# Optimization experiments

Measured on AMD Instinct MI355X. Metric: run time of the kernel, lower is better.

Reference implementation:

```python
import jax, jax.numpy as jnp
import numpy as np

B, T, I, H = 64, 512, 512, 1024

def _xavier(key, shape):
    fan_in, fan_out = shape
    limit = float(np.sqrt(6.0 / (fan_in + fan_out)))
    return jax.random.uniform(key, shape, jnp.float32, -limit, limit)

def setup_inputs() -> dict:
    key = jax.random.key(0)
    ks = jax.random.split(key, 9)
    inp = {
        'x': jax.random.normal(ks[0], (B, T, I), jnp.float32),
        'U_inputgate': _xavier(ks[1], (I, H)),
        'V_inputgate': _xavier(ks[2], (H, H)),
        'bias_inputgate': jnp.zeros((H,), jnp.float32),
        'U_forget': _xavier(ks[3], (I, H)),
        'V_forget': _xavier(ks[4], (H, H)),
        'bias_forget': jnp.zeros((H,), jnp.float32),
        'U_tilded': _xavier(ks[5], (I, H)),
        'V_tilded': _xavier(ks[6], (H, H)),
        'bias_tilded': jnp.zeros((H,), jnp.float32),
        'U_output': _xavier(ks[7], (I, H)),
        'V_output': _xavier(ks[8], (H, H)),
        'bias_output': jnp.zeros((H,), jnp.float32),
    }
    return inp

def reference(x, U_inputgate, V_inputgate, bias_inputgate,
              U_forget, V_forget, bias_forget,
              U_tilded, V_tilded, bias_tilded,
              U_output, V_output, bias_output):
    batch = x.shape[0]
    hidden = V_inputgate.shape[0]
    # Precompute input projections for all timesteps (fused gate GEMM):
    # concat U's -> one [I, 4H] GEMM over the whole sequence.
    U = jnp.concatenate([U_inputgate, U_forget, U_tilded, U_output], axis=1)  # [I, 4H]
    V = jnp.concatenate([V_inputgate, V_forget, V_tilded, V_output], axis=1)  # [H, 4H]
    b = jnp.concatenate([bias_inputgate, bias_forget, bias_tilded, bias_output])  # [4H]
    xU = jnp.einsum('bti,ig->btg', x, U) + b  # [B, T, 4H]

    def step(carry, xu_t):
        h, c = carry
        g = xu_t + h @ V  # [B, 4H]
        i_g = jax.nn.sigmoid(g[:, :hidden])
        f_g = jax.nn.sigmoid(g[:, hidden:2 * hidden])
        c_t = jnp.tanh(g[:, 2 * hidden:3 * hidden])
        o_g = jax.nn.sigmoid(g[:, 3 * hidden:])
        c_new = i_g * c_t + f_g * c
        h_new = o_g * jnp.tanh(c_new)
        return (h_new, c_new), None

    h0 = jnp.zeros((batch, hidden), x.dtype)
    c0 = jnp.zeros((batch, hidden), x.dtype)
    (h_t, c_t), _ = jax.lax.scan(step, (h0, c0), jnp.swapaxes(xU, 0, 1))
    return (h_t, c_t)
```

## Files before the change

### kernel.cpp

```cpp
#include <hip/hip_runtime.h>
#include <hip/hip_bf16.h>
#include <cstdio>
#include <cstdint>

#define BB 64
#define TT 512
#define II 512
#define HH 1024
#define G4H 4096
#define TC 256

typedef __attribute__((ext_vector_type(8))) short short8b;
typedef __attribute__((ext_vector_type(4))) float f32x4;
typedef unsigned long long ull;

union U16 { uint4 u; short8b s; };

#define AT_LD32(p)   __hip_atomic_load((p), __ATOMIC_RELAXED, __HIP_MEMORY_SCOPE_AGENT)
#define AT_LD64(p)   __hip_atomic_load((p), __ATOMIC_RELAXED, __HIP_MEMORY_SCOPE_AGENT)
#define AT_ST32(p,v) __hip_atomic_store((p), (v), __ATOMIC_RELAXED, __HIP_MEMORY_SCOPE_AGENT)
#define AT_ST64(p,v) __hip_atomic_store((p), (v), __ATOMIC_RELAXED, __HIP_MEMORY_SCOPE_AGENT)

__device__ __forceinline__ ushort f2bf(float f) {
    union { float f; unsigned u; } x; x.f = f;
    unsigned r = x.u + 0x7FFFu + ((x.u >> 16) & 1u);
    return (ushort)(r >> 16);
}
__device__ __forceinline__ float bf2f(ushort b) {
    union { unsigned u; float f; } x; x.u = ((unsigned)b) << 16;
    return x.f;
}
__device__ __forceinline__ float sigm(float x) { return 1.f / (1.f + __expf(-x)); }
__device__ __forceinline__ float tanh_(float x) { return 2.f / (1.f + __expf(-2.f * x)) - 1.f; }

__global__ void conv_f32_bf16(const float* __restrict__ in, ushort* __restrict__ out, int n) {
    int i = (blockIdx.x * blockDim.x + threadIdx.x) * 4;
    int stride = gridDim.x * blockDim.x * 4;
    for (; i < n; i += stride) {
        float4 v = *(const float4*)(in + i);
        ushort4 o;
        o.x = f2bf(v.x); o.y = f2bf(v.y); o.z = f2bf(v.z); o.w = f2bf(v.w);
        *(ushort4*)(out + i) = o;
    }
}

__global__ void transpose_bf16(const float* __restrict__ in, ushort* __restrict__ out, int K) {
    __shared__ float tile[32][33];
    int j0 = blockIdx.x * 32;
    int k0 = blockIdx.y * 32;
    int tx = threadIdx.x, ty = threadIdx.y;
    #pragma unroll
    for (int i = 0; i < 32; i += 8)
        tile[ty + i][tx] = in[(size_t)(k0 + ty + i) * 1024 + j0 + tx];
    __syncthreads();
    #pragma unroll
    for (int i = 0; i < 32; i += 8)
        out[(size_t)(j0 + ty + i) * K + k0 + tx] = f2bf(tile[tx][ty + i]);
}

__global__ __launch_bounds__(256) void gemm_xu(
    const ushort* __restrict__ A, const ushort* __restrict__ Bt,
    const float* __restrict__ b0, const float* __restrict__ b1,
    const float* __restrict__ b2, const float* __restrict__ b3,
    ushort* __restrict__ C, int t0)
{
    __shared__ ushort As[128 * 64];
    __shared__ ushort Bs[128 * 64];
    const int m0 = blockIdx.x * 128;
    const int n0 = blockIdx.y * 128;
    const int tid = threadIdx.x;
    const int lane = tid & 63;
    const int wave = tid >> 6;
    const int wm = (wave >> 1) * 64;
    const int wn = (wave & 1) * 64;
    const int kgrp = lane >> 4;

    const ushort* Abase = A + ((size_t)(m0 >> 8) * TT + t0 + (m0 & 255)) * 512;

    f32x4 acc[4][4];
    #pragma unroll
    for (int i = 0; i < 4; ++i)
        #pragma unroll
        for (int j = 0; j < 4; ++j) acc[i][j] = (f32x4){0.f, 0.f, 0.f, 0.f};

    for (int k0 = 0; k0 < 512; k0 += 64) {
        __syncthreads();
        #pragma unroll
        for (int p = 0; p < 4; ++p) {
            int idx = p * 256 + tid;
            int row = idx >> 3;
            int kc  = idx & 7;
            uint4 va = *(const uint4*)(Abase + (size_t)row * 512 + k0 + kc * 8);
            uint4 vb = *(const uint4*)(Bt + (size_t)(n0 + row) * 512 + k0 + kc * 8);
            int bo = (row * 128 + kc * 16) ^ ((row & 7) << 4);
            *(uint4*)((char*)As + bo) = va;
            *(uint4*)((char*)Bs + bo) = vb;
        }
        __syncthreads();
        #pragma unroll
        for (int ks = 0; ks < 2; ++ks) {
            U16 af[4], bfr[4];
            #pragma unroll
            for (int i = 0; i < 4; ++i) {
                int row = wm + i * 16 + (lane & 15);
                int ao = (row * 128 + ks * 64 + kgrp * 16) ^ ((row & 7) << 4);
                af[i].u = *(const uint4*)((const char*)As + ao);
                int col = wn + i * 16 + (lane & 15);
                int bo = (col * 128 + ks * 64 + kgrp * 16) ^ ((col & 7) << 4);
                bfr[i].u = *(const uint4*)((const char*)Bs + bo);
            }
            #pragma unroll
            for (int i = 0; i < 4; ++i)
                #pragma unroll
                for (int j = 0; j < 4; ++j)
                    acc[i][j] = __builtin_amdgcn_mfma_f32_16x16x32_bf16(af[i].s, bfr[j].s, acc[i][j], 0, 0, 0);
        }
    }
    #pragma unroll
    for (int i = 0; i < 4; ++i) {
        #pragma unroll
        for (int j = 0; j < 4; ++j) {
            int row = m0 + wm + i * 16 + (lane >> 4) * 4;
            int col = n0 + wn + j * 16 + (lane & 15);
            int gate = col >> 10;
            const float* bp = (gate == 0) ? b0 : (gate == 1) ? b1 : (gate == 2) ? b2 : b3;
            float bias = bp[col & 1023];
            #pragma unroll
            for (int r = 0; r < 4; ++r)
                C[(size_t)(row + r) * G4H + col] = f2bf(acc[i][j][r] + bias);
        }
    }
}

__global__ __launch_bounds__(256, 1) void lstm_rec(
    const ushort* __restrict__ xU,
    const ushort* __restrict__ V_t,
    char* __restrict__ hb,
    float* __restrict__ cbuf,
    float* __restrict__ out,
    unsigned* __restrict__ flags,
    int t0)
{
    __shared__ __align__(16) ushort Vl[64 * 1024];
    __shared__ __align__(16) ushort hl[16 * 1024];

    const int wgid = blockIdx.x;
    const int grp = wgid >> 6;
    const int slice = wgid & 63;
    const int tid = threadIdx.x;
    const int lane = tid & 63;
    const int w = tid >> 6;

    #pragma unroll
    for (int p = 0; p < 32; ++p) {
        int idx = p * 256 + tid;
        int c  = idx >> 7;
        int kc = idx & 127;
        int colg = (c & 3) * 1024 + slice * 16 + ((c >> 4) << 2) + ((c >> 2) & 3);
        uint4 v = *(const uint4*)(V_t + (size_t)colg * 1024 + kc * 8);
        int bo = (c * 2048 + kc * 16) ^ ((c & 7) << 4);
        *(uint4*)((char*)Vl + bo) = v;
    }

    const int myrow = (lane >> 4) * 4 + (lane & 3);
    const int mycol = 4 * w + ((lane >> 2) & 3);
    const int growf = grp * 16 + myrow;
    const int hcol = slice * 16 + mycol;
    float c_reg = (t0 == 0) ? 0.f : cbuf[(size_t)growf * 1024 + hcol];

    const int kgrp = lane >> 4;
    const int lrow = lane & 15;
    const int arow_sw = (lrow & 7) << 4;
    const int bc = w * 16 + (lane & 15);
    const int bxor = (bc & 7) << 4;
    const int bo_base = bc * 2048 + kgrp * 16;

    __syncthreads();

    for (int t = t0; t < t0 + TC; ++t) {
        size_t xbase = ((size_t)growf * TC + (t - t0)) * G4H + hcol;
        ushort xi = xU[xbase], xf = xU[xbase + 1024], xc = xU[xbase + 2048], xo = xU[xbase + 3072];

        if (tid < 64) {
            const unsigned tgt = (unsigned)t;
            const unsigned* f = flags + grp * 64;
            while (!__all((int)(AT_LD32(&f[tid]) >= tgt)))
                __builtin_amdgcn_s_sleep(1);
            asm volatile("" ::: "memory");
        }
        __syncthreads();

        {
            const char* hsrc = hb + (size_t)(t & 1) * 131072 + grp * 32768;
            ull vv[16];
            #pragma unroll
            for (int it = 0; it < 16; ++it)
                vv[it] = AT_LD64((const ull*)(hsrc + (size_t)(it * 256 + tid) * 8));
            #pragma unroll
            for (int it = 0; it < 16; ++it) {
                int q = it * 256 + tid;
                int row = q >> 8;
                int cb  = (q & 255) * 8;
                *(ull*)((char*)hl + ((row * 2048 + cb) ^ ((row & 7) << 4))) = vv[it];
            }
        }
        __syncthreads();

        f32x4 acc0 = (f32x4){0.f,0.f,0.f,0.f}, acc1 = (f32x4){0.f,0.f,0.f,0.f};
        const char* hlb = (const char*)hl;
        #pragma unroll
        for (int ks = 0; ks < 32; ks += 2) {
            U16 a0, b0, a1, b1;
            a0.u = *(const uint4*)(hlb + ((lrow * 2048 + (ks * 4 + kgrp) * 16) ^ arow_sw));
            b0.u = *(const uint4*)((const char*)Vl + ((bo_base + ks * 64) ^ bxor));
            acc0 = __builtin_amdgcn_mfma_f32_16x16x32_bf16(a0.s, b0.s, acc0, 0, 0, 0);
            a1.u = *(const uint4*)(hlb + ((lrow * 2048 + (ks * 4 + 4 + kgrp) * 16) ^ arow_sw));
            b1.u = *(const uint4*)((const char*)Vl + ((bo_base + ks * 64 + 64) ^ bxor));
            acc1 = __builtin_amdgcn_mfma_f32_16x16x32_bf16(a1.s, b1.s, acc1, 0, 0, 0);
        }
        float a0 = acc0[0] + acc1[0], a1 = acc0[1] + acc1[1];
        float a2 = acc0[2] + acc1[2], a3 = acc0[3] + acc1[3];

        {
            float b0 = __shfl_xor(a1, 1), b1 = __shfl_xor(a0, 1);
            float b2 = __shfl_xor(a3, 1), b3 = __shfl_xor(a2, 1);
            bool o1 = (lane & 1) != 0;
            a0 = o1 ? b0 : a0;  a1 = o1 ? a1 : b1;
            a2 = o1 ? b2 : a2;  a3 = o1 ? a3 : b3;
            b0 = __shfl_xor(a2, 2); b1 = __shfl_xor(a3, 2);
            b2 = __shfl_xor(a0, 2); b3 = __shfl_xor(a1, 2);
            bool o2 = (lane & 2) != 0;
            a0 = o2 ? b0 : a0;  a1 = o2 ? b1 : a1;
            a2 = o2 ? a2 : b2;  a3 = o2 ? a3 : b3;
        }

        float gi = a0 + bf2f(xi), gf = a1 + bf2f(xf);
        float gc = a2 + bf2f(xc), go = a3 + bf2f(xo);
        float ig = sigm(gi), fg = sigm(gf), ct = tanh_(gc), og = sigm(go);
        c_reg = ig * ct + fg * c_reg;
        float h = og * tanh_(c_reg);
        ushort hbf = f2bf(h);
        unsigned h1 = __shfl_down((unsigned)hbf, 4);
        unsigned h2 = __shfl_down((unsigned)hbf, 8);
        unsigned h3 = __shfl_down((unsigned)hbf, 12);
        if (((lane >> 2) & 3) == 0) {
            ull pk = (ull)hbf | ((ull)(h1 & 0xffff) << 16)
                   | ((ull)(h2 & 0xffff) << 32) | ((ull)(h3 & 0xffff) << 48);
            AT_ST64((ull*)(hb + (size_t)((t & 1) ^ 1) * 131072 + grp * 32768
                           + myrow * 2048 + (size_t)(slice * 16 + 4 * w) * 2), pk);
        }
        if (t == TT - 1) {
            out[(size_t)growf * 1024 + hcol] = h;
            out[(size_t)BB * HH + (size_t)growf * 1024 + hcol] = c_reg;
        }
        __syncthreads();
        if (tid == 0) AT_ST32(flags + grp * 64 + slice, (unsigned)(t + 1));
    }

    if (t0 + TC < TT)
        cbuf[(size_t)growf * 1024 + hcol] = c_reg;
}

extern "C" void kernel_launch(void* const* d_in, const int* in_sizes, int n_in,
                              void* d_out, int out_size, void* d_ws, size_t ws_size,
                              hipStream_t stream) {
    const float* x = (const float*)d_in[0];
    const float* U[4] = {(const float*)d_in[1], (const float*)d_in[4], (const float*)d_in[7], (const float*)d_in[10]};
    const float* V[4] = {(const float*)d_in[2], (const float*)d_in[5], (const float*)d_in[8], (const float*)d_in[11]};
    const float* bias[4] = {(const float*)d_in[3], (const float*)d_in[6], (const float*)d_in[9], (const float*)d_in[12]};
    float* out = (float*)d_out;

    const size_t x_elems = (size_t)BB * TT * II;
    size_t off = 0;
    auto alloc = [&](size_t bytes) { size_t o = off; off = (off + bytes + 255) & ~(size_t)255; return o; };
    size_t o_xbf   = alloc(x_elems * 2);
    size_t o_Ut    = alloc((size_t)G4H * II * 2);
    size_t o_Vt    = alloc((size_t)G4H * HH * 2);
    size_t o_xU    = alloc((size_t)BB * TC * G4H * 2);
    size_t o_hbuf  = alloc(262144);
    size_t o_cbuf  = alloc((size_t)BB * HH * 4);
    size_t o_flags = alloc(4 * 64 * 4);
    if (ws_size < off) {
        fprintf(stderr, "kernel_launch: ws too small: need %zu have %zu\n", off, ws_size);
        return;
    }
    char* ws = (char*)d_ws;
    ushort* x_bf = (ushort*)(ws + o_xbf);
    ushort* U_t  = (ushort*)(ws + o_Ut);
    ushort* V_t  = (ushort*)(ws + o_Vt);
    ushort* xU   = (ushort*)(ws + o_xU);
    char*   hbuf = ws + o_hbuf;
    float*  cbuf = (float*)(ws + o_cbuf);
    unsigned* flags = (unsigned*)(ws + o_flags);

    hipMemsetAsync(flags, 0, 4 * 64 * 4, stream);
    hipMemsetAsync(hbuf, 0, 262144, stream);

    conv_f32_bf16<<<4096, 256, 0, stream>>>(x, x_bf, (int)x_elems);

    for (int g = 0; g < 4; ++g)
        transpose_bf16<<<dim3(32, 16), dim3(32, 8), 0, stream>>>(U[g], U_t + (size_t)g * 1024 * 512, 512);
    for (int g = 0; g < 4; ++g)
        transpose_bf16<<<dim3(32, 32), dim3(32, 8), 0, stream>>>(V[g], V_t + (size_t)g * 1024 * 1024, 1024);

    for (int c = 0; c < TT / TC; ++c) {
        int t0 = c * TC;
        gemm_xu<<<dim3(128, 32), 256, 0, stream>>>(x_bf, U_t, bias[0], bias[1], bias[2], bias[3], xU, t0);
        lstm_rec<<<256, 256, 0, stream>>>(xU, V_t, hbuf, cbuf, out, flags, t0);
    }
}
```

Measured before the change: 2.109 ms.

## Fuse prep kernels and pad per-slice flags to separate cache lines

Merges the x conversion and the eight weight-transpose launches into one prep kernel to cut launch overhead. In the recurrent loop, every wavefront now polls the step flags itself instead of only the first wave followed by a block barrier. Each flag is padded to 64 bytes so pollers and writers no longer share cache lines. This removes one __syncthreads per timestep but multiplies polling traffic by the number of waves.

```diff
diff --git a/kernel.cpp b/kernel.cpp
--- a/kernel.cpp
+++ b/kernel.cpp
@@ -33,22 +33,45 @@
 __device__ __forceinline__ float sigm(float x) { return 1.f / (1.f + __expf(-x)); }
 __device__ __forceinline__ float tanh_(float x) { return 2.f / (1.f + __expf(-2.f * x)) - 1.f; }
 
-__global__ void conv_f32_bf16(const float* __restrict__ in, ushort* __restrict__ out, int n) {
-    int i = (blockIdx.x * blockDim.x + threadIdx.x) * 4;
-    int stride = gridDim.x * blockDim.x * 4;
-    for (; i < n; i += stride) {
-        float4 v = *(const float4*)(in + i);
-        ushort4 o;
-        o.x = f2bf(v.x); o.y = f2bf(v.y); o.z = f2bf(v.z); o.w = f2bf(v.w);
-        *(ushort4*)(out + i) = o;
-    }
-}
-
-__global__ void transpose_bf16(const float* __restrict__ in, ushort* __restrict__ out, int K) {
+__global__ __launch_bounds__(256) void prep_fused(
+    const float* __restrict__ x, ushort* __restrict__ x_bf,
+    const float* __restrict__ U0, const float* __restrict__ U1,
+    const float* __restrict__ U2, const float* __restrict__ U3,
+    ushort* __restrict__ U_t,
+    const float* __restrict__ V0, const float* __restrict__ V1,
+    const float* __restrict__ V2, const float* __restrict__ V3,
+    ushort* __restrict__ V_t)
+{
     __shared__ float tile[32][33];
-    int j0 = blockIdx.x * 32;
-    int k0 = blockIdx.y * 32;
-    int tx = threadIdx.x, ty = threadIdx.y;
+    const int b = blockIdx.x;
+    const int tid = threadIdx.x;
+    if (b < 2048) {
+        int i = (b * 256 + tid) * 4;
+        const int n = BB * TT * II;
+        const int stride = 2048 * 256 * 4;
+        for (; i < n; i += stride) {
+            float4 v = *(const float4*)(x + i);
+            ushort4 o;
+            o.x = f2bf(v.x); o.y = f2bf(v.y); o.z = f2bf(v.z); o.w = f2bf(v.w);
+            *(ushort4*)(x_bf + i) = o;
+        }
+        return;
+    }
+    const int tx = tid & 31, ty = tid >> 5;
+    const float* in; ushort* out; int K, j0, k0;
+    if (b < 4096) {
+        int u = b - 2048;
+        int g = u >> 9, r = u & 511;
+        const float* Us[4] = {U0, U1, U2, U3};
+        in = Us[g]; out = U_t + (size_t)g * 1024 * 512; K = 512;
+        j0 = (r & 31) * 32; k0 = (r >> 5) * 32;
+    } else {
+        int v = b - 4096;
+        int g = v >> 10, r = v & 1023;
+        const float* Vs[4] = {V0, V1, V2, V3};
+        in = Vs[g]; out = V_t + (size_t)g * 1024 * 1024; K = 1024;
+        j0 = (r & 31) * 32; k0 = (r >> 5) * 32;
+    }
     #pragma unroll
     for (int i = 0; i < 32; i += 8)
         tile[ty + i][tx] = in[(size_t)(k0 + ty + i) * 1024 + j0 + tx];
@@ -181,21 +204,22 @@
         size_t xbase = ((size_t)growf * TC + (t - t0)) * G4H + hcol;
         ushort xi = xU[xbase], xf = xU[xbase + 1024], xc = xU[xbase + 2048], xo = xU[xbase + 3072];
 
-        if (tid < 64) {
+        {
             const unsigned tgt = (unsigned)t;
-            const unsigned* f = flags + grp * 64;
-            while (!__all((int)(AT_LD32(&f[tid]) >= tgt)))
+            const unsigned* f = flags + grp * 1024;
+            while (!__all((int)(AT_LD32(&f[lane * 16]) >= tgt)))
                 __builtin_amdgcn_s_sleep(1);
             asm volatile("" ::: "memory");
         }
-        __syncthreads();
-
+
+        ull vv[16];
         {
             const char* hsrc = hb + (size_t)(t & 1) * 131072 + grp * 32768;
-            ull vv[16];
             #pragma unroll
             for (int it = 0; it < 16; ++it)
                 vv[it] = AT_LD64((const ull*)(hsrc + (size_t)(it * 256 + tid) * 8));
+        }
+        {
             #pragma unroll
             for (int it = 0; it < 16; ++it) {
                 int q = it * 256 + tid;
@@ -254,7 +278,7 @@
             out[(size_t)BB * HH + (size_t)growf * 1024 + hcol] = c_reg;
         }
         __syncthreads();
-        if (tid == 0) AT_ST32(flags + grp * 64 + slice, (unsigned)(t + 1));
+        if (tid == 0) AT_ST32(flags + grp * 1024 + slice * 16, (unsigned)(t + 1));
     }
 
     if (t0 + TC < TT)
@@ -279,7 +303,7 @@
     size_t o_xU    = alloc((size_t)BB * TC * G4H * 2);
     size_t o_hbuf  = alloc(262144);
     size_t o_cbuf  = alloc((size_t)BB * HH * 4);
-    size_t o_flags = alloc(4 * 64 * 4);
+    size_t o_flags = alloc(4 * 64 * 64);
     if (ws_size < off) {
         fprintf(stderr, "kernel_launch: ws too small: need %zu have %zu\n", off, ws_size);
         return;
@@ -293,15 +317,12 @@
     float*  cbuf = (float*)(ws + o_cbuf);
     unsigned* flags = (unsigned*)(ws + o_flags);
 
-    hipMemsetAsync(flags, 0, 4 * 64 * 4, stream);
+    hipMemsetAsync(flags, 0, 4 * 64 * 64, stream);
     hipMemsetAsync(hbuf, 0, 262144, stream);
 
-    conv_f32_bf16<<<4096, 256, 0, stream>>>(x, x_bf, (int)x_elems);
-
-    for (int g = 0; g < 4; ++g)
-        transpose_bf16<<<dim3(32, 16), dim3(32, 8), 0, stream>>>(U[g], U_t + (size_t)g * 1024 * 512, 512);
-    for (int g = 0; g < 4; ++g)
-        transpose_bf16<<<dim3(32, 32), dim3(32, 8), 0, stream>>>(V[g], V_t + (size_t)g * 1024 * 1024, 1024);
+    prep_fused<<<8192, 256, 0, stream>>>(x, x_bf,
+        U[0], U[1], U[2], U[3], U_t,
+        V[0], V[1], V[2], V[3], V_t);
 
     for (int c = 0; c < TT / TC; ++c) {
         int t0 = c * TC;
```

Result: faster. 1.892 ms (median of 2 runs) (-10.3%).
